# Performance work log

Hardware: AMD Instinct MI355X
Metric: run time of the kernel (lower is better)

The kernel has to match this reference:

```python
import jax, jax.numpy as jnp
import numpy as np

DT = 0.2
DX = 0.0327249  # 2*pi/192
KPAD = 2  # (kernel_size-1)//2 for 5x5 periodic 'same' padding
# total derivative order of fd00, fd01, fd10, fd02, fd11, fd20
_ORD = np.array([0, 1, 1, 2, 2, 2], dtype=np.float32)
_SCALES = (DX ** -_ORD)  # FD2d scale = dx^-(jx+jy)


def _poly_apply(w0, b0, w1, b1, wf, bf, x):
    # SymNet (expr.poly): each hidden layer computes two linear combos and
    # appends their product as a new channel; final linear -> scalar.
    o = x @ w0.T + b0                                        # [..., 2]
    x = jnp.concatenate([x, o[..., :1] * o[..., 1:2]], -1)   # [..., 13]
    o = x @ w1.T + b1
    x = jnp.concatenate([x, o[..., :1] * o[..., 1:2]], -1)   # [..., 14]
    return (x @ wf.T + bf)[..., 0]


def _rhs(u, kernels, pw0, pb0, pw1, pb1, pwf, pbf):
    # u: [B, C, H, W]
    B, C, H, W = u.shape
    ks = kernels * jnp.asarray(_SCALES, u.dtype)[:, None, None]   # [6,5,5]
    k01f = -ks[1, :, ::-1]   # -flip along width  (torch flip([3]))
    k10f = -ks[2, ::-1, :]   # -flip along height (torch flip([2]))
    kall = jnp.concatenate([ks, k01f[None], k10f[None]], 0)[:, None]  # [8,1,5,5]
    up = jnp.pad(u, ((0, 0), (0, 0), (KPAD, KPAD), (KPAD, KPAD)), mode='wrap')
    up = up.reshape(B * C, 1, H + 2 * KPAD, W + 2 * KPAD)
    D = jax.lax.conv_general_dilated(up, kall, (1, 1), 'VALID')   # [B*C,8,H,W]
    D = D.reshape(B, C, 8, H, W)
    # per-channel blocks ordered (00,01,10,02,11,20)
    base = jnp.transpose(D[:, :, :6], (0, 3, 4, 1, 2)).reshape(B, H, W, C * 6)
    f01 = jnp.transpose(D[:, :, 6], (0, 2, 3, 1))   # [B,H,W,C]
    f10 = jnp.transpose(D[:, :, 7], (0, 2, 3, 1))
    # upwind: pick normal vs flipped 1st-order stencil by sign of d(poly_k)/d(u01/u10)
    Xsel = base
    for k in range(C):
        pk = (pw0[k], pb0[k], pw1[k], pb1[k], pwf[k], pbf[k])
        G = jax.grad(lambda z: _poly_apply(*pk, z).sum())(base)   # [B,H,W,C*6]
        g01, g10 = G[..., k * 6 + 1], G[..., k * 6 + 2]
        u01 = jnp.where(g01 > 0, base[..., k * 6 + 1], f01[..., k])
        u10 = jnp.where(g10 > 0, base[..., k * 6 + 2], f10[..., k])
        Xsel = Xsel.at[..., k * 6 + 1].set(u01).at[..., k * 6 + 2].set(u10)
    uadd = jnp.stack(
        [_poly_apply(pw0[k], pb0[k], pw1[k], pb1[k], pwf[k], pbf[k], Xsel)
         for k in range(C)], axis=1)                              # [B,C,H,W]
    return uadd


def setup_inputs() -> dict:
    key = jax.random.key(0)
    ks = jax.random.split(key, 8)
    f32 = jnp.float32
    inp = {
        'init': jax.random.normal(ks[0], (16, 2, 192, 192), f32),
        'kernels': jax.random.normal(ks[1], (6, 5, 5), f32) * 0.002,
        'poly_w0': jax.random.normal(ks[2], (2, 2, 12), f32) * 0.01,
        'poly_b0': jax.random.normal(ks[3], (2, 2), f32) * 0.01,
        'poly_w1': jax.random.normal(ks[4], (2, 2, 13), f32) * 0.01,
        'poly_b1': jax.random.normal(ks[5], (2, 2), f32) * 0.01,
        'poly_wf': jax.random.normal(ks[6], (2, 1, 14), f32) * 0.01,
        'poly_bf': jax.random.normal(ks[7], (2, 1), f32) * 0.01,
        'T': 1,
    }
    return inp


def reference(init, kernels, poly_w0, poly_b0, poly_w1, poly_b1, poly_wf, poly_bf, T):
    stepnum = int(round(T / DT))  # 5 RK2 (midpoint) steps
    u = init
    for _ in range(stepnum):
        uh = u + (DT / 2) * _rhs(u, kernels, poly_w0, poly_b0, poly_w1, poly_b1, poly_wf, poly_bf)
        u = u + DT * _rhs(uh, kernels, poly_w0, poly_b0, poly_w1, poly_b1, poly_wf, poly_bf)
    return u
```

## Files before the change

### kernel.cpp

```cpp
#include <hip/hip_runtime.h>

typedef float v2f __attribute__((ext_vector_type(2)));

#define HH 192
#define WW 192
#define BATCH 16
#define PLANE (HH*WW)
#define NELEM (BATCH*2*PLANE)

#define TILEX 32
#define TILEY 8
#define SW 36
#define SH2 12
#define NSITE (SH2*SW)

__global__ void prep_kernel(const float* __restrict__ kern,
                            const float* __restrict__ pw0, const float* __restrict__ pb0,
                            const float* __restrict__ pw1, const float* __restrict__ pb1,
                            const float* __restrict__ pwf, const float* __restrict__ pbf,
                            float* __restrict__ ws)
{
    int t = blockIdx.x * blockDim.x + threadIdx.x;
    if (t < 200) {
        const float inv  = 1.0f / 0.0327249f;
        const float inv2 = inv * inv;
        const float sc[6] = {1.0f, inv, inv, inv2, inv2, inv2};
        int o = t / 8, j = t % 8, dy = o / 5, dx = o % 5;
        float v;
        if (j < 6)       v =  kern[j*25 + dy*5 + dx] * sc[j];
        else if (j == 6) v = -kern[1*25 + dy*5 + (4-dx)] * sc[1];
        else             v = -kern[2*25 + (4-dy)*5 + dx] * sc[2];
        ws[o*8 + j] = v;
    } else if (t < 279) {
        int p = t - 200;
        int arr, a, b;
        if (p < 12)       { arr=0; a=p;      b=24+p; }
        else if (p < 24)  { int i=p-12; arr=0; a=12+i; b=36+i; }
        else if (p == 24) { arr=1; a=0; b=2; }
        else if (p == 25) { arr=1; a=1; b=3; }
        else if (p < 38)  { int i=p-26; arr=2; a=i;    b=26+i; }
        else if (p < 50)  { int i=p-38; arr=2; a=13+i; b=39+i; }
        else if (p == 50) { arr=2; a=12; b=38; }
        else if (p == 51) { arr=2; a=25; b=51; }
        else if (p == 52) { arr=3; a=0; b=2; }
        else if (p == 53) { arr=3; a=1; b=3; }
        else if (p < 68)  { int i=p-54; arr=4; a=i; b=14+i; }
        else if (p == 68) { arr=5; a=0; b=1; }
        else {
            const signed char   A0[10] = {1,2,13,14,1,2,14,15,1,2};
            const signed char   A1[10] = {31,32,43,44,33,34,46,47,21,22};
            const unsigned char AR[10] = {0,0,0,0,2,2,2,2,4,4};
            int i = p - 69; arr = AR[i]; a = A0[i]; b = A1[i];
        }
        const float* bases[6] = {pw0, pb0, pw1, pb1, pwf, pbf};
        v2f v; v[0] = bases[arr][a]; v[1] = bases[arr][b];
        ((v2f*)(ws + 256))[p] = v;
    }
}

__global__ __launch_bounds__(128, 5) void rhs_kernel(
    const float* __restrict__ uin,
    const float* __restrict__ ubase,
    float* __restrict__ uout,
    const float* __restrict__ ws,
    float alpha)
{
    const float* K8T = ws;
    const v2f* PP = (const v2f*)(ws + 256);

    __shared__ v2f sh[SH2][SW];
    const int b   = blockIdx.z;
    const int ty0 = blockIdx.y * TILEY;
    const int tx0 = blockIdx.x * TILEX;
    const int tid = threadIdx.x;
    const size_t bo = (size_t)b * 2 * PLANE;

    const float* uin_b = uin + bo;
    for (int i = tid; i < NSITE; i += 128) {
        const int ly  = i / SW;
        const int col = i - ly * SW;
        int gy = ty0 + ly - 2;  if (gy < 0) gy += HH; else if (gy >= HH) gy -= HH;
        int gx = tx0 + col - 2; if (gx < 0) gx += WW; else if (gx >= WW) gx -= WW;
        const int gi = gy*WW + gx;
        v2f v; v[0] = uin_b[gi]; v[1] = uin_b[PLANE + gi];
        sh[ly][col] = v;
    }
    __syncthreads();

    const int cy = tid >> 4;
    const int x2 = (tid & 15) * 2;

    v2f D2[2][8];
    #pragma unroll
    for (int p = 0; p < 2; ++p)
        #pragma unroll
        for (int j = 0; j < 8; ++j)
            D2[p][j] = (v2f){0.0f, 0.0f};

    #pragma unroll 1
    for (int dy = 0; dy < 5; ++dy) {
        v2f row[6];
        #pragma unroll
        for (int dx = 0; dx < 6; ++dx)
            row[dx] = sh[cy + dy][x2 + dx];
        const float* Kt = K8T + dy * 40;
        #pragma unroll
        for (int dx = 0; dx < 5; ++dx) {
            #pragma unroll
            for (int j = 0; j < 8; ++j) {
                const float w = Kt[dx*8 + j];
                D2[0][j] += row[dx]   * w;
                D2[1][j] += row[dx+1] * w;
            }
        }
    }

#define Z(p,i) (D2[p][(i)%6][(i)/6])

    v2f res[2];
    #pragma unroll
    for (int p = 0; p < 2; ++p) {
        v2f o0 = PP[24], o1 = PP[25];
        #pragma unroll
        for (int i = 0; i < 12; ++i) {
            const float zv = Z(p, i);
            o0 += PP[i]    * zv;
            o1 += PP[12+i] * zv;
        }
        const v2f pb = o0 * o1;
        v2f q0 = PP[52] + PP[50]*pb;
        v2f q1 = PP[53] + PP[51]*pb;
        #pragma unroll
        for (int i = 0; i < 12; ++i) {
            const float zv = Z(p, i);
            q0 += PP[26+i] * zv;
            q1 += PP[38+i] * zv;
        }

        const v2f t1 = o1*PP[69] + o0*PP[71];
        const v2f g1 = PP[77] + PP[66]*t1
            + PP[67]*(q1*(PP[73] + PP[50]*t1) + q0*(PP[75] + PP[51]*t1));
        const v2f t2 = o1*PP[70] + o0*PP[72];
        const v2f g2 = PP[78] + PP[66]*t2
            + PP[67]*(q1*(PP[74] + PP[50]*t2) + q0*(PP[76] + PP[51]*t2));

        const float s1 = (g1[0] > 0.0f) ? Z(p,1) : D2[p][6][0];
        const float s2 = (g2[0] > 0.0f) ? Z(p,2) : D2[p][7][0];
        const float s3 = (g1[1] > 0.0f) ? Z(p,7) : D2[p][6][1];
        const float s4 = (g2[1] > 0.0f) ? Z(p,8) : D2[p][7][1];
#define XV(i) ((i)==1 ? s1 : (i)==2 ? s2 : (i)==7 ? s3 : (i)==8 ? s4 : Z(p,(i)))

        v2f f0 = PP[24], f1 = PP[25];
        #pragma unroll
        for (int i = 0; i < 12; ++i) {
            const float xv = XV(i);
            f0 += PP[i]    * xv;
            f1 += PP[12+i] * xv;
        }
        const v2f pf = f0 * f1;
        v2f r0 = PP[52] + PP[50]*pf;
        v2f r1 = PP[53] + PP[51]*pf;
        v2f y  = PP[68] + PP[66]*pf;
        #pragma unroll
        for (int i = 0; i < 12; ++i) {
            const float xv = XV(i);
            r0 += PP[26+i] * xv;
            r1 += PP[38+i] * xv;
            y  += PP[54+i] * xv;
        }
        res[p] = y + PP[67]*(r0*r1);
#undef XV
    }

    const int oy = ty0 + cy, ox = tx0 + x2;
    const size_t o0i = bo + (size_t)oy * WW + ox;
    const float2 base0 = *(const float2*)(ubase + o0i);
    const float2 base1 = *(const float2*)(ubase + o0i + PLANE);
    float2 r0, r1;
    r0.x = base0.x + alpha * res[0][0];
    r0.y = base0.y + alpha * res[1][0];
    r1.x = base1.x + alpha * res[0][1];
    r1.y = base1.y + alpha * res[1][1];
    *(float2*)(uout + o0i)         = r0;
    *(float2*)(uout + o0i + PLANE) = r1;
}

extern "C" void kernel_launch(void* const* d_in, const int* in_sizes, int n_in,
                              void* d_out, int out_size, void* d_ws, size_t ws_size,
                              hipStream_t stream)
{
    const float* init = (const float*)d_in[0];
    const float* kern = (const float*)d_in[1];
    const float* pw0  = (const float*)d_in[2];
    const float* pb0  = (const float*)d_in[3];
    const float* pw1  = (const float*)d_in[4];
    const float* pb1  = (const float*)d_in[5];
    const float* pwf  = (const float*)d_in[6];
    const float* pbf  = (const float*)d_in[7];
    float* out = (float*)d_out;
    float* ws  = (float*)d_ws;

    float* bufA = ws + 512;
    float* bufH = bufA + NELEM;

    prep_kernel<<<dim3(1), dim3(320), 0, stream>>>(kern, pw0, pb0, pw1, pb1, pwf, pbf, ws);

    const dim3 grid(WW/TILEX, HH/TILEY, BATCH);
    const dim3 block(128);
    const float DTF = 0.2f, DTH = 0.1f;

    rhs_kernel<<<grid, block, 0, stream>>>(init, init, bufH, ws, DTH);
    rhs_kernel<<<grid, block, 0, stream>>>(bufH, init, bufA, ws, DTF);
    for (int s = 0; s < 3; ++s) {
        rhs_kernel<<<grid, block, 0, stream>>>(bufA, bufA, bufH, ws, DTH);
        rhs_kernel<<<grid, block, 0, stream>>>(bufH, bufA, bufA, ws, DTF);
    }
    rhs_kernel<<<grid, block, 0, stream>>>(bufA, bufA, bufH, ws, DTH);
    rhs_kernel<<<grid, block, 0, stream>>>(bufH, bufA, out,  ws, DTF);
}
```

Before: 219.0 us.

## Widen tile to 96 columns, vectorize halo loads, reuse shared tile for base

Triples the tile width to 96 columns with 384-thread blocks, which shrinks the share of halo overhead per tile. The shared-memory fill now loads float2 pairs from each channel plane and interleaves them with a single float4 store. When the base input equals the stencil input, it reads the centre values from shared memory instead of reloading them from global memory. The trade-off is fewer blocks in the grid (2x24x16) and more shared memory per block, which may lower occupancy.

```diff
diff --git a/kernel.cpp b/kernel.cpp
--- a/kernel.cpp
+++ b/kernel.cpp
@@ -8,11 +8,11 @@
 #define PLANE (HH*WW)
 #define NELEM (BATCH*2*PLANE)
 
-#define TILEX 32
+#define TILEX 96
 #define TILEY 8
-#define SW 36
+#define SW 100
 #define SH2 12
-#define NSITE (SH2*SW)
+#define NPAIR 600
 
 __global__ void prep_kernel(const float* __restrict__ kern,
                             const float* __restrict__ pw0, const float* __restrict__ pb0,
@@ -58,7 +58,7 @@
     }
 }
 
-__global__ __launch_bounds__(128, 5) void rhs_kernel(
+__global__ __launch_bounds__(384, 4) void rhs_kernel(
     const float* __restrict__ uin,
     const float* __restrict__ ubase,
     float* __restrict__ uout,
@@ -76,19 +76,22 @@
     const size_t bo = (size_t)b * 2 * PLANE;
 
     const float* uin_b = uin + bo;
-    for (int i = tid; i < NSITE; i += 128) {
-        const int ly  = i / SW;
-        const int col = i - ly * SW;
+    for (int i = tid; i < NPAIR; i += 384) {
+        const int ly  = i / 50;
+        const int cp  = i - ly * 50;
+        const int col = cp * 2;
         int gy = ty0 + ly - 2;  if (gy < 0) gy += HH; else if (gy >= HH) gy -= HH;
-        int gx = tx0 + col - 2; if (gx < 0) gx += WW; else if (gx >= WW) gx -= WW;
-        const int gi = gy*WW + gx;
-        v2f v; v[0] = uin_b[gi]; v[1] = uin_b[PLANE + gi];
-        sh[ly][col] = v;
+        int gx0 = tx0 + col - 2; if (gx0 < 0) gx0 += WW; else if (gx0 >= WW) gx0 -= WW;
+        const int gi = gy*WW + gx0;
+        const float2 a = *(const float2*)(uin_b + gi);
+        const float2 c = *(const float2*)(uin_b + PLANE + gi);
+        float4 st; st.x = a.x; st.y = c.x; st.z = a.y; st.w = c.y;
+        *(float4*)&sh[ly][col] = st;
     }
     __syncthreads();
 
-    const int cy = tid >> 4;
-    const int x2 = (tid & 15) * 2;
+    const int cy = tid / 48;
+    const int x2 = (tid - cy * 48) * 2;
 
     v2f D2[2][8];
     #pragma unroll
@@ -174,8 +177,16 @@
 
     const int oy = ty0 + cy, ox = tx0 + x2;
     const size_t o0i = bo + (size_t)oy * WW + ox;
-    const float2 base0 = *(const float2*)(ubase + o0i);
-    const float2 base1 = *(const float2*)(ubase + o0i + PLANE);
+    float2 base0, base1;
+    if (ubase == uin) {
+        const v2f c0 = sh[cy+2][x2+2];
+        const v2f c1 = sh[cy+2][x2+3];
+        base0.x = c0[0]; base0.y = c1[0];
+        base1.x = c0[1]; base1.y = c1[1];
+    } else {
+        base0 = *(const float2*)(ubase + o0i);
+        base1 = *(const float2*)(ubase + o0i + PLANE);
+    }
     float2 r0, r1;
     r0.x = base0.x + alpha * res[0][0];
     r0.y = base0.y + alpha * res[1][0];
@@ -206,7 +217,7 @@
     prep_kernel<<<dim3(1), dim3(320), 0, stream>>>(kern, pw0, pb0, pw1, pb1, pwf, pbf, ws);
 
     const dim3 grid(WW/TILEX, HH/TILEY, BATCH);
-    const dim3 block(128);
+    const dim3 block(384);
     const float DTF = 0.2f, DTH = 0.1f;
 
     rhs_kernel<<<grid, block, 0, stream>>>(init, init, bufH, ws, DTH);
```

After: 242.1 us. +10.5%, slower.
